# Kernel tuning notes

Measured on AMD Instinct MI355X. Metric: run time of the kernel, lower is better.

The kernel has to match this reference:

```python
import jax, jax.numpy as jnp
import numpy as np
import math

N_NODES = 64000
N_GRAPHS = 512
HIDDEN = 128
CLUSTERS = 10
NUM_FILTER = 16
N_CLASSES = 2
S_HID = math.ceil((HIDDEN + CLUSTERS) / 2)  # 69
P_HID = 8


def _mlp2(x, w1, b1, w2, b2):
    # 2-layer MLP: Linear -> ReLU -> Linear (matches MLP(2, in, hid, out))
    return jax.nn.relu(x @ w1 + b1) @ w2 + b2


def setup_inputs() -> dict:
    key = jax.random.key(0)
    ks = jax.random.split(key, 12)
    # node embeddings (output of get_emb)
    H_all = jax.random.normal(ks[0], (N_NODES, HIDDEN), dtype=jnp.float32)
    # graph indicator: 125 nodes per graph, sorted (as produced by batching)
    batch = jnp.repeat(jnp.arange(N_GRAPHS, dtype=jnp.int32), N_NODES // N_GRAPHS)
    targets = jax.random.randint(ks[1], (N_GRAPHS,), 0, N_CLASSES, dtype=jnp.int32)
    s = 0.05
    # S_mlp: hidden -> S_HID -> clusters
    w1 = jax.random.normal(ks[2], (HIDDEN, S_HID), dtype=jnp.float32) * s
    b1 = jnp.zeros((S_HID,), dtype=jnp.float32)
    w2 = jax.random.normal(ks[3], (S_HID, CLUSTERS), dtype=jnp.float32) * s
    b2 = jnp.zeros((CLUSTERS,), dtype=jnp.float32)
    # final: hidden*clusters -> 2
    wf = jax.random.normal(ks[4], (HIDDEN * CLUSTERS, N_CLASSES), dtype=jnp.float32) * s
    bf = jnp.zeros((N_CLASSES,), dtype=jnp.float32)
    # prototype_features_MLP: hidden -> 8 -> num_graph_filter
    p1 = jax.random.normal(ks[5], (HIDDEN, P_HID), dtype=jnp.float32) * s
    pb1 = jnp.zeros((P_HID,), dtype=jnp.float32)
    p2 = jax.random.normal(ks[6], (P_HID, NUM_FILTER), dtype=jnp.float32) * s
    pb2 = jnp.zeros((NUM_FILTER,), dtype=jnp.float32)
    # correlation parameters (initialized like the torch module)
    corr_inter = jax.nn.softmax(jax.random.uniform(ks[7], (N_CLASSES, NUM_FILTER)), axis=0)
    corr_intra = jax.nn.softmax(jax.random.uniform(ks[8], (N_CLASSES, NUM_FILTER)), axis=1)
    return {"H_all": H_all, "batch": batch, "targets": targets,
            "w1": w1, "b1": b1, "w2": w2, "b2": b2,
            "wf": wf, "bf": bf,
            "p1": p1, "pb1": pb1, "p2": p2, "pb2": pb2,
            "corr_inter": corr_inter, "corr_intra": corr_intra}


def reference(H_all, batch, targets, w1, b1, w2, b2, wf, bf,
              p1, pb1, p2, pb2, corr_inter, corr_intra):
    # per-node soft cluster assignment  [N, C]
    S_all = jax.nn.softmax(_mlp2(H_all, w1, b1, w2, b2), axis=-1)
    # segment matmul E_g = S_g^T @ H_g  -> [B, C, D] via segment-reduced outer products
    outer = S_all[:, :, None] * H_all[:, None, :]  # [N, C, D]
    E_all = jax.ops.segment_sum(outer, batch, num_segments=N_GRAPHS)
    B = E_all.shape[0]
    pred1 = E_all.reshape(B, -1) @ wf + bf  # dropout off (eval)
    p = jax.nn.softmax(pred1, axis=-1)
    # multinomial sample from pred_softmax (no grad)
    key = jax.random.key(42)
    sample = jax.random.categorical(key, jnp.log(jax.lax.stop_gradient(p) + 1e-12), axis=-1)
    ind_positive_sample = sample == targets
    oh = jax.nn.one_hot(sample, N_CLASSES, dtype=p.dtype)
    epsilon = jax.lax.stop_gradient(jnp.where(oh != 0, 1.0 - p, -p))
    sample_cat_oh = p + epsilon  # straight-through one-hot
    Q = jax.nn.softmax(_mlp2(E_all, p1, pb1, p2, pb2), axis=-1)  # [B, C, F]
    correlation = jax.nn.softmax(corr_inter, axis=0) * jax.nn.softmax(corr_intra, axis=1)  # [2, F]
    correlation_mask = sample_cat_oh @ correlation  # [B, F]
    feature_mask = jnp.sum(Q * correlation_mask[:, None, :], axis=-1)  # [B, C]
    E_masked = feature_mask[:, :, None] * E_all  # einsum('bi,bij->bij')
    pred2 = E_masked.reshape(B, -1) @ wf + bf
    return (pred1, pred2, ind_positive_sample, S_all, E_all, Q)
```

## Files before the change

### kernel.cpp

```cpp
#include <hip/hip_runtime.h>

#define NN 64000
#define NG 512
#define NPG 125
#define DIM 128
#define NC 10
#define SHID 69
#define NF 16
#define PHID 8
#define ELPAD 132
#define TSTR 85
#define PSTR 41

#define OFF_PRED1 0
#define OFF_PRED2 1024
#define OFF_IND   2048
#define OFF_S     2560
#define OFF_E     642560
#define OFF_Q     1297920

typedef __attribute__((ext_vector_type(8))) short short8;
typedef __attribute__((ext_vector_type(4))) float f32x4;

__device__ __forceinline__ unsigned rotl32(unsigned x, int r) {
    return (x << r) | (x >> (32 - r));
}

__device__ __forceinline__ void threefry_0_42(unsigned x0, unsigned x1,
                                              unsigned& o0, unsigned& o1) {
    const unsigned k0 = 0u, k1 = 42u;
    const unsigned k2 = k0 ^ k1 ^ 0x1BD11BDAu;
    unsigned ks[3] = {k0, k1, k2};
    const int R0[4] = {13, 15, 26, 6};
    const int R1[4] = {17, 29, 16, 24};
    x0 += k0; x1 += k1;
    #pragma unroll
    for (int i = 0; i < 5; i++) {
        const int* R = (i & 1) ? R1 : R0;
        #pragma unroll
        for (int r = 0; r < 4; r++) {
            x0 += x1;
            x1 = rotl32(x1, R[r]);
            x1 ^= x0;
        }
        x0 += ks[(i + 1) % 3];
        x1 += ks[(i + 2) % 3] + (unsigned)(i + 1);
    }
    o0 = x0; o1 = x1;
}

__device__ __forceinline__ unsigned random_bits_partitionable(unsigned i) {
    unsigned o0, o1;
    threefry_0_42(0u, i, o0, o1);
    return o0 ^ o1;
}

__device__ __forceinline__ float gumbel_from_bits(unsigned bits) {
    float f = __uint_as_float((bits >> 9) | 0x3f800000u) - 1.0f;
    if (f <= 0.0f) f = 1.1754943508222875e-38f;
    return -logf(-logf(f));
}

#define R10(M) M(0) M(1) M(2) M(3) M(4) M(5) M(6) M(7) M(8) M(9)

__global__ __launch_bounds__(256, 4) void k_node_mlp(
    const float* __restrict__ H, const float* __restrict__ w1,
    const float* __restrict__ b1, const float* __restrict__ w2,
    const float* __restrict__ b2, float* __restrict__ S) {
    __shared__ __align__(16) char lds[40960];
    short* fragHi = (short*)lds;
    short* fragLo = (short*)(lds + 20480);
    int tid = threadIdx.x;

    for (int s = tid; s < 1280; s += 256) {
        int jt = s >> 8, ks = (s >> 6) & 3, l = s & 63;
        int j = jt * 16 + (l & 15);
        int kb = ks * 32 + ((l >> 4) & 3) * 8;
        short8 vh, vl;
        #pragma unroll
        for (int i = 0; i < 8; i++) {
            float x = (j < SHID) ? w1[(kb + i) * SHID + j] : 0.0f;
            unsigned u = __float_as_uint(x);
            vh[i] = (short)(u >> 16);
            float hf = __uint_as_float(u & 0xFFFF0000u);
            float lo = x - hf;
            vl[i] = (short)(__float_as_uint(lo) >> 16);
        }
        *(short8*)(fragHi + (size_t)s * 8) = vh;
        *(short8*)(fragLo + (size_t)s * 8) = vl;
    }
    __syncthreads();

    int w = tid >> 6, l = tid & 63;
    int node = blockIdx.x * 64 + w * 16 + (l & 15);
    const float* Hp = H + (size_t)node * DIM + ((l >> 4) & 3) * 8;

    short8 aHi[4], aLo[4];
    #pragma unroll
    for (int ks = 0; ks < 4; ks++) {
        float4 x0 = *(const float4*)(Hp + ks * 32);
        float4 x1 = *(const float4*)(Hp + ks * 32 + 4);
        float xs[8] = {x0.x, x0.y, x0.z, x0.w, x1.x, x1.y, x1.z, x1.w};
        #pragma unroll
        for (int i = 0; i < 8; i++) {
            unsigned u = __float_as_uint(xs[i]);
            aHi[ks][i] = (short)(u >> 16);
            float lo = xs[i] - __uint_as_float(u & 0xFFFF0000u);
            aLo[ks][i] = (short)(__float_as_uint(lo) >> 16);
        }
    }

    f32x4 acc[5];
    #pragma unroll
    for (int jt = 0; jt < 5; jt++) {
        f32x4 a = {0.f, 0.f, 0.f, 0.f};
        #pragma unroll
        for (int ks = 0; ks < 4; ks++) {
            int slot = (jt * 4 + ks) * 64 + l;
            short8 bh = *(short8*)(fragHi + (size_t)slot * 8);
            short8 bl = *(short8*)(fragLo + (size_t)slot * 8);
            a = __builtin_amdgcn_mfma_f32_16x16x32_bf16(aHi[ks], bh, a, 0, 0, 0);
            a = __builtin_amdgcn_mfma_f32_16x16x32_bf16(aLo[ks], bh, a, 0, 0, 0);
            a = __builtin_amdgcn_mfma_f32_16x16x32_bf16(aHi[ks], bl, a, 0, 0, 0);
        }
        acc[jt] = a;
    }
    __syncthreads();

    float* Ts = (float*)lds;
    float* Ps = (float*)(lds + 21760);
    #pragma unroll
    for (int jt = 0; jt < 5; jt++) {
        int j = jt * 16 + (l & 15);
        float bj = (j < SHID) ? b1[j] : 0.0f;
        #pragma unroll
        for (int r = 0; r < 4; r++) {
            int m = w * 16 + ((l >> 4) & 3) * 4 + r;
            float tv = acc[jt][r];
            Ts[m * TSTR + j] = (j < SHID) ? fmaxf(tv + bj, 0.0f) : 0.0f;
        }
    }
    __syncthreads();

    {
        int n = tid & 63, q = tid >> 6;
        float lg[NC] = {};
        for (int jj = 0; jj < 18; jj++) {
            int j = q * 18 + jj;
            int jx = (j < SHID) ? j : (SHID - 1);
            float tr = Ts[n * TSTR + j];
            const float* w2r = w2 + jx * NC;
            #pragma unroll
            for (int c = 0; c < NC; c++) lg[c] = fmaf(tr, w2r[c], lg[c]);
        }
        #pragma unroll
        for (int c = 0; c < NC; c++) Ps[n * PSTR + q * NC + c] = lg[c];
    }
    __syncthreads();

    if (tid < 64) {
        int n = tid;
        const float* pr = &Ps[n * PSTR];
        #define LD(c) float s##c = pr[c] + pr[10 + c] + pr[20 + c] + pr[30 + c] + b2[c];
        R10(LD)
        #undef LD
        float m = fmaxf(fmaxf(fmaxf(s0, s1), fmaxf(s2, s3)),
                        fmaxf(fmaxf(fmaxf(s4, s5), fmaxf(s6, s7)), fmaxf(s8, s9)));
        float e0 = expf(s0 - m), e1 = expf(s1 - m), e2 = expf(s2 - m),
              e3 = expf(s3 - m), e4 = expf(s4 - m), e5 = expf(s5 - m),
              e6 = expf(s6 - m), e7 = expf(s7 - m), e8 = expf(s8 - m),
              e9 = expf(s9 - m);
        float ssum = ((e0 + e1) + (e2 + e3)) + ((e4 + e5) + (e6 + e7)) + (e8 + e9);
        float inv = 1.0f / ssum;
        float2* Sp2 = (float2*)(S + ((size_t)blockIdx.x * 64 + n) * NC);
        Sp2[0] = make_float2(e0 * inv, e1 * inv);
        Sp2[1] = make_float2(e2 * inv, e3 * inv);
        Sp2[2] = make_float2(e4 * inv, e5 * inv);
        Sp2[3] = make_float2(e6 * inv, e7 * inv);
        Sp2[4] = make_float2(e8 * inv, e9 * inv);
    }
}

__global__ __launch_bounds__(512, 2) void k_E_tail(
    const float* __restrict__ H, const float* __restrict__ S,
    const float* __restrict__ wf, const float* __restrict__ bf,
    const int* __restrict__ targets,
    const float* __restrict__ p1, const float* __restrict__ pb1,
    const float* __restrict__ p2, const float* __restrict__ pb2,
    const float* __restrict__ ci, const float* __restrict__ cr,
    float* __restrict__ E, float* __restrict__ pred1, float* __restrict__ pred2,
    float* __restrict__ ind, float* __restrict__ Q) {
    __shared__ __align__(8) float Sl[128 * NC];
    __shared__ float Epart[3 * 128 * NC];
    __shared__ __align__(16) float El[NC * ELPAD];
    __shared__ float fmbuf[NC];
    int g = blockIdx.x, tid = threadIdx.x;

    const float* Sg = S + (size_t)g * NPG * NC;
    for (int i = tid; i < 128 * NC; i += 512) Sl[i] = (i < NPG * NC) ? Sg[i] : 0.0f;
    __syncthreads();

    int q = tid >> 7;
    int d = tid & 127;
    const float* Hg = H + (size_t)g * NPG * DIM + d;

    #define DECLA(c) float a##c = 0.f;
    R10(DECLA)
    #undef DECLA
    int n0 = q * 32;
    #pragma unroll
    for (int ib = 0; ib < 32; ib += 4) {
        float h[4];
        #pragma unroll
        for (int u = 0; u < 4; u++) {
            int nh = min(n0 + ib + u, NPG - 1);
            h[u] = Hg[(size_t)nh * DIM];
        }
        #pragma unroll
        for (int u = 0; u < 4; u++) {
            const float2* S2 = (const float2*)(Sl + (n0 + ib + u) * NC);
            float2 s01 = S2[0], s23 = S2[1], s45 = S2[2], s67 = S2[3], s89 = S2[4];
            a0 = fmaf(s01.x, h[u], a0); a1 = fmaf(s01.y, h[u], a1);
            a2 = fmaf(s23.x, h[u], a2); a3 = fmaf(s23.y, h[u], a3);
            a4 = fmaf(s45.x, h[u], a4); a5 = fmaf(s45.y, h[u], a5);
            a6 = fmaf(s67.x, h[u], a6); a7 = fmaf(s67.y, h[u], a7);
            a8 = fmaf(s89.x, h[u], a8); a9 = fmaf(s89.y, h[u], a9);
        }
    }
    if (q > 0) {
        float* ep = &Epart[(q - 1) * 128 * NC + d * NC];
        #define STP(c) ep[c] = a##c;
        R10(STP)
        #undef STP
    }
    __syncthreads();
    if (q == 0) {
        const float* e1p = &Epart[d * NC];
        const float* e2p = &Epart[128 * NC + d * NC];
        const float* e3p = &Epart[2 * 128 * NC + d * NC];
        float* Eo = E + (size_t)g * (NC * DIM) + d;
        #define CMB(c) { a##c += e1p[c] + e2p[c] + e3p[c]; \
                         El[c * ELPAD + d] = a##c; Eo[c * DIM] = a##c; }
        R10(CMB)
        #undef CMB
    }
    __syncthreads();

    const float2* wf2 = (const float2*)wf;
    int l = tid;
    int samp = 0;
    float corr_lf = 0.f;

    if (tid < 64) {
        if (l < 32) {
            int i = l >> 4, f = l & 15;
            float a = ci[f], b = ci[NF + f];
            float mm = fmaxf(a, b);
            float ea = expf(a - mm), eb = expf(b - mm);
            float inter = expf(ci[i * NF + f] - mm) / (ea + eb);
            float mi = -1e30f;
            for (int j = 0; j < NF; j++) mi = fmaxf(mi, cr[i * NF + j]);
            float ri = 0.f;
            for (int j = 0; j < NF; j++) ri += expf(cr[i * NF + j] - mi);
            float intra = expf(cr[i * NF + f] - mi) / ri;
            corr_lf = inter * intra;
        }

        float a0 = 0.f, a1 = 0.f;
        #pragma unroll
        for (int i = 0; i < 20; i++) {
            int idx = i * 64 + l;
            float e = El[(idx >> 7) * ELPAD + (idx & 127)];
            float2 w = wf2[idx];
            a0 = fmaf(e, w.x, a0);
            a1 = fmaf(e, w.y, a1);
        }
        #pragma unroll
        for (int off = 32; off > 0; off >>= 1) {
            a0 += __shfl_down(a0, off);
            a1 += __shfl_down(a1, off);
        }
        if (l == 0) {
            float y0 = a0 + bf[0], y1 = a1 + bf[1];
            pred1[g * 2] = y0;
            pred1[g * 2 + 1] = y1;
            float m = fmaxf(y0, y1);
            float e0 = expf(y0 - m), e1 = expf(y1 - m), s = e0 + e1;
            float p0 = e0 / s, pp1 = e1 / s;
            float g0 = gumbel_from_bits(random_bits_partitionable(2 * g));
            float g1 = gumbel_from_bits(random_bits_partitionable(2 * g + 1));
            float l0 = logf(p0 + 1e-12f) + g0;
            float l1 = logf(pp1 + 1e-12f) + g1;
            samp = (l1 > l0) ? 1 : 0;
            ind[g] = (samp == targets[g]) ? 1.0f : 0.0f;
        }
        samp = __shfl(samp, 0);

        if (l < 40) {
            int p = l >> 2, s = l & 3;
            float ua = pb1[2 * s], ub = pb1[2 * s + 1];
            const float4* E4 = (const float4*)&El[p * ELPAD];
            #pragma unroll 4
            for (int k4 = 0; k4 < 32; k4++) {
                float4 e4 = E4[k4];
                float es[4] = {e4.x, e4.y, e4.z, e4.w};
                #pragma unroll
                for (int kk = 0; kk < 4; kk++) {
                    int k = k4 * 4 + kk;
                    ua = fmaf(es[kk], p1[k * PHID + 2 * s], ua);
                    ub = fmaf(es[kk], p1[k * PHID + 2 * s + 1], ub);
                }
            }
            ua = fmaxf(ua, 0.f);
            ub = fmaxf(ub, 0.f);
            float v[NF];
            #pragma unroll
            for (int f = 0; f < NF; f++) {
                v[f] = pb2[f] * 0.25f;
                v[f] = fmaf(ua, p2[(2 * s) * NF + f], v[f]);
                v[f] = fmaf(ub, p2[(2 * s + 1) * NF + f], v[f]);
            }
            #pragma unroll
            for (int f = 0; f < NF; f++) {
                v[f] += __shfl_xor(v[f], 1);
                v[f] += __shfl_xor(v[f], 2);
            }
            float m = v[0];
            #pragma unroll
            for (int f = 1; f < NF; f++) m = fmaxf(m, v[f]);
            float ssum = 0.f, qv[NF];
            #pragma unroll
            for (int f = 0; f < NF; f++) { qv[f] = expf(v[f] - m); ssum += qv[f]; }
            float inv = 1.0f / ssum;
            #pragma unroll
            for (int f = 0; f < NF; f++) qv[f] *= inv;
            float* Qo = Q + ((size_t)g * NC + p) * NF;
            ((float4*)Qo)[s] = make_float4(qv[s * 4], qv[s * 4 + 1], qv[s * 4 + 2], qv[s * 4 + 3]);
            float fmv = 0.f;
            #pragma unroll
            for (int f = 0; f < NF; f++) {
                float cv = __shfl(corr_lf, samp * NF + f);
                fmv = fmaf(qv[f], cv, fmv);
            }
            if (s == 0) fmbuf[p] = fmv;
        }
    }
    __syncthreads();

    if (tid < 64) {
        float b0 = 0.f, b1acc = 0.f;
        #pragma unroll
        for (int i = 0; i < 20; i++) {
            int idx = i * 64 + l;
            float e = El[(idx >> 7) * ELPAD + (idx & 127)] * fmbuf[idx >> 7];
            float2 w = wf2[idx];
            b0 = fmaf(e, w.x, b0);
            b1acc = fmaf(e, w.y, b1acc);
        }
        #pragma unroll
        for (int off = 32; off > 0; off >>= 1) {
            b0 += __shfl_down(b0, off);
            b1acc += __shfl_down(b1acc, off);
        }
        if (l == 0) {
            pred2[g * 2] = b0 + bf[0];
            pred2[g * 2 + 1] = b1acc + bf[1];
        }
    }
}

extern "C" void kernel_launch(void* const* d_in, const int* in_sizes, int n_in,
                              void* d_out, int out_size, void* d_ws, size_t ws_size,
                              hipStream_t stream) {
    const float* H       = (const float*)d_in[0];
    const int*   targets = (const int*)d_in[2];
    const float* w1      = (const float*)d_in[3];
    const float* b1      = (const float*)d_in[4];
    const float* w2      = (const float*)d_in[5];
    const float* b2      = (const float*)d_in[6];
    const float* wf      = (const float*)d_in[7];
    const float* bf      = (const float*)d_in[8];
    const float* p1      = (const float*)d_in[9];
    const float* pb1     = (const float*)d_in[10];
    const float* p2      = (const float*)d_in[11];
    const float* pb2     = (const float*)d_in[12];
    const float* ci      = (const float*)d_in[13];
    const float* cr      = (const float*)d_in[14];

    float* out   = (float*)d_out;
    float* pred1 = out + OFF_PRED1;
    float* pred2 = out + OFF_PRED2;
    float* ind   = out + OFF_IND;
    float* S     = out + OFF_S;
    float* E     = out + OFF_E;
    float* Q     = out + OFF_Q;

    k_node_mlp<<<NN / 64, 256, 0, stream>>>(H, w1, b1, w2, b2, S);
    k_E_tail<<<NG, 512, 0, stream>>>(H, S, wf, bf, targets, p1, pb1, p2, pb2,
                                     ci, cr, E, pred1, pred2, ind, Q);
}
```

Measured before the change: 126.9 us.

## Fuse node MLP with per-graph segment sum and precompute split w1 fragments

Merges the per-node S MLP kernel into the per-graph kernel so each block computes S for its 125 nodes, keeps S in LDS, and then forms E without re-reading S from global memory. The bf16 hi/lo split of w1 now runs once in a small pre-kernel that writes to workspace, and each block copies the prepared fragments into LDS. This removes the S round trip and one launch gap, and H is reused across both phases. In exchange, blocks shrink from 512 to 256 threads, LDS per block grows, occupancy drops, and the pre-kernel adds a launch.

```diff
diff --git a/kernel.cpp b/kernel.cpp
--- a/kernel.cpp
+++ b/kernel.cpp
@@ -9,8 +9,8 @@
 #define NF 16
 #define PHID 8
 #define ELPAD 132
-#define TSTR 85
-#define PSTR 41
+#define TSTR 81
+#define PSTR 21
 
 #define OFF_PRED1 0
 #define OFF_PRED2 1024
@@ -63,191 +63,221 @@
 
 #define R10(M) M(0) M(1) M(2) M(3) M(4) M(5) M(6) M(7) M(8) M(9)
 
-__global__ __launch_bounds__(256, 4) void k_node_mlp(
-    const float* __restrict__ H, const float* __restrict__ w1,
+__global__ void k_split_w1(const float* __restrict__ w1, short* __restrict__ ws) {
+    int e = blockIdx.x * 256 + threadIdx.x;
+    int slot = e >> 3, i = e & 7;
+    int jt = slot >> 8, ks = (slot >> 6) & 3, l = slot & 63;
+    int j = jt * 16 + (l & 15);
+    int kb = ks * 32 + ((l >> 4) & 3) * 8;
+    float x = (j < SHID) ? w1[(kb + i) * SHID + j] : 0.0f;
+    unsigned u = __float_as_uint(x);
+    short hi = (short)(u >> 16);
+    float hf = __uint_as_float(u & 0xFFFF0000u);
+    short lo = (short)(__float_as_uint(x - hf) >> 16);
+    ws[e] = hi;
+    ws[10240 + e] = lo;
+}
+
+__global__ __launch_bounds__(256, 2) void k_fused(
+    const float* __restrict__ H, const short* __restrict__ ws,
     const float* __restrict__ b1, const float* __restrict__ w2,
-    const float* __restrict__ b2, float* __restrict__ S) {
-    __shared__ __align__(16) char lds[40960];
-    short* fragHi = (short*)lds;
-    short* fragLo = (short*)(lds + 20480);
-    int tid = threadIdx.x;
-
-    for (int s = tid; s < 1280; s += 256) {
-        int jt = s >> 8, ks = (s >> 6) & 3, l = s & 63;
-        int j = jt * 16 + (l & 15);
-        int kb = ks * 32 + ((l >> 4) & 3) * 8;
-        short8 vh, vl;
-        #pragma unroll
-        for (int i = 0; i < 8; i++) {
-            float x = (j < SHID) ? w1[(kb + i) * SHID + j] : 0.0f;
-            unsigned u = __float_as_uint(x);
-            vh[i] = (short)(u >> 16);
-            float hf = __uint_as_float(u & 0xFFFF0000u);
-            float lo = x - hf;
-            vl[i] = (short)(__float_as_uint(lo) >> 16);
-        }
-        *(short8*)(fragHi + (size_t)s * 8) = vh;
-        *(short8*)(fragLo + (size_t)s * 8) = vl;
-    }
-    __syncthreads();
-
-    int w = tid >> 6, l = tid & 63;
-    int node = blockIdx.x * 64 + w * 16 + (l & 15);
-    const float* Hp = H + (size_t)node * DIM + ((l >> 4) & 3) * 8;
-
-    short8 aHi[4], aLo[4];
-    #pragma unroll
-    for (int ks = 0; ks < 4; ks++) {
-        float4 x0 = *(const float4*)(Hp + ks * 32);
-        float4 x1 = *(const float4*)(Hp + ks * 32 + 4);
-        float xs[8] = {x0.x, x0.y, x0.z, x0.w, x1.x, x1.y, x1.z, x1.w};
-        #pragma unroll
-        for (int i = 0; i < 8; i++) {
-            unsigned u = __float_as_uint(xs[i]);
-            aHi[ks][i] = (short)(u >> 16);
-            float lo = xs[i] - __uint_as_float(u & 0xFFFF0000u);
-            aLo[ks][i] = (short)(__float_as_uint(lo) >> 16);
-        }
-    }
-
-    f32x4 acc[5];
-    #pragma unroll
-    for (int jt = 0; jt < 5; jt++) {
-        f32x4 a = {0.f, 0.f, 0.f, 0.f};
-        #pragma unroll
-        for (int ks = 0; ks < 4; ks++) {
-            int slot = (jt * 4 + ks) * 64 + l;
-            short8 bh = *(short8*)(fragHi + (size_t)slot * 8);
-            short8 bl = *(short8*)(fragLo + (size_t)slot * 8);
-            a = __builtin_amdgcn_mfma_f32_16x16x32_bf16(aHi[ks], bh, a, 0, 0, 0);
-            a = __builtin_amdgcn_mfma_f32_16x16x32_bf16(aLo[ks], bh, a, 0, 0, 0);
-            a = __builtin_amdgcn_mfma_f32_16x16x32_bf16(aHi[ks], bl, a, 0, 0, 0);
-        }
-        acc[jt] = a;
-    }
-    __syncthreads();
-
-    float* Ts = (float*)lds;
-    float* Ps = (float*)(lds + 21760);
-    #pragma unroll
-    for (int jt = 0; jt < 5; jt++) {
-        int j = jt * 16 + (l & 15);
-        float bj = (j < SHID) ? b1[j] : 0.0f;
-        #pragma unroll
-        for (int r = 0; r < 4; r++) {
-            int m = w * 16 + ((l >> 4) & 3) * 4 + r;
-            float tv = acc[jt][r];
-            Ts[m * TSTR + j] = (j < SHID) ? fmaxf(tv + bj, 0.0f) : 0.0f;
-        }
-    }
-    __syncthreads();
-
-    {
-        int n = tid & 63, q = tid >> 6;
-        float lg[NC] = {};
-        for (int jj = 0; jj < 18; jj++) {
-            int j = q * 18 + jj;
-            int jx = (j < SHID) ? j : (SHID - 1);
-            float tr = Ts[n * TSTR + j];
-            const float* w2r = w2 + jx * NC;
-            #pragma unroll
-            for (int c = 0; c < NC; c++) lg[c] = fmaf(tr, w2r[c], lg[c]);
-        }
-        #pragma unroll
-        for (int c = 0; c < NC; c++) Ps[n * PSTR + q * NC + c] = lg[c];
-    }
-    __syncthreads();
-
-    if (tid < 64) {
-        int n = tid;
-        const float* pr = &Ps[n * PSTR];
-        #define LD(c) float s##c = pr[c] + pr[10 + c] + pr[20 + c] + pr[30 + c] + b2[c];
-        R10(LD)
-        #undef LD
-        float m = fmaxf(fmaxf(fmaxf(s0, s1), fmaxf(s2, s3)),
-                        fmaxf(fmaxf(fmaxf(s4, s5), fmaxf(s6, s7)), fmaxf(s8, s9)));
-        float e0 = expf(s0 - m), e1 = expf(s1 - m), e2 = expf(s2 - m),
-              e3 = expf(s3 - m), e4 = expf(s4 - m), e5 = expf(s5 - m),
-              e6 = expf(s6 - m), e7 = expf(s7 - m), e8 = expf(s8 - m),
-              e9 = expf(s9 - m);
-        float ssum = ((e0 + e1) + (e2 + e3)) + ((e4 + e5) + (e6 + e7)) + (e8 + e9);
-        float inv = 1.0f / ssum;
-        float2* Sp2 = (float2*)(S + ((size_t)blockIdx.x * 64 + n) * NC);
-        Sp2[0] = make_float2(e0 * inv, e1 * inv);
-        Sp2[1] = make_float2(e2 * inv, e3 * inv);
-        Sp2[2] = make_float2(e4 * inv, e5 * inv);
-        Sp2[3] = make_float2(e6 * inv, e7 * inv);
-        Sp2[4] = make_float2(e8 * inv, e9 * inv);
-    }
-}
-
-__global__ __launch_bounds__(512, 2) void k_E_tail(
-    const float* __restrict__ H, const float* __restrict__ S,
+    const float* __restrict__ b2,
     const float* __restrict__ wf, const float* __restrict__ bf,
     const int* __restrict__ targets,
     const float* __restrict__ p1, const float* __restrict__ pb1,
     const float* __restrict__ p2, const float* __restrict__ pb2,
     const float* __restrict__ ci, const float* __restrict__ cr,
-    float* __restrict__ E, float* __restrict__ pred1, float* __restrict__ pred2,
+    float* __restrict__ S, float* __restrict__ E,
+    float* __restrict__ pred1, float* __restrict__ pred2,
     float* __restrict__ ind, float* __restrict__ Q) {
-    __shared__ __align__(8) float Sl[128 * NC];
-    __shared__ float Epart[3 * 128 * NC];
-    __shared__ __align__(16) float El[NC * ELPAD];
-    __shared__ float fmbuf[NC];
+    __shared__ __align__(16) char lds[57600];
     int g = blockIdx.x, tid = threadIdx.x;
 
-    const float* Sg = S + (size_t)g * NPG * NC;
-    for (int i = tid; i < 128 * NC; i += 512) Sl[i] = (i < NPG * NC) ? Sg[i] : 0.0f;
-    __syncthreads();
-
-    int q = tid >> 7;
-    int d = tid & 127;
-    const float* Hg = H + (size_t)g * NPG * DIM + d;
-
-    #define DECLA(c) float a##c = 0.f;
-    R10(DECLA)
-    #undef DECLA
-    int n0 = q * 32;
+    {
+        const float4* src = (const float4*)ws;
+        float4* dst = (float4*)lds;
+        #pragma unroll
+        for (int k = 0; k < 10; k++) dst[k * 256 + tid] = src[k * 256 + tid];
+    }
+    short* fragHi = (short*)lds;
+    short* fragLo = (short*)(lds + 20480);
+    __syncthreads();
+
+    int w = tid >> 6, l = tid & 63;
+
+    short8 aHi[2][4], aLo[2][4];
     #pragma unroll
-    for (int ib = 0; ib < 32; ib += 4) {
-        float h[4];
-        #pragma unroll
-        for (int u = 0; u < 4; u++) {
-            int nh = min(n0 + ib + u, NPG - 1);
-            h[u] = Hg[(size_t)nh * DIM];
-        }
-        #pragma unroll
-        for (int u = 0; u < 4; u++) {
-            const float2* S2 = (const float2*)(Sl + (n0 + ib + u) * NC);
-            float2 s01 = S2[0], s23 = S2[1], s45 = S2[2], s67 = S2[3], s89 = S2[4];
-            a0 = fmaf(s01.x, h[u], a0); a1 = fmaf(s01.y, h[u], a1);
-            a2 = fmaf(s23.x, h[u], a2); a3 = fmaf(s23.y, h[u], a3);
-            a4 = fmaf(s45.x, h[u], a4); a5 = fmaf(s45.y, h[u], a5);
-            a6 = fmaf(s67.x, h[u], a6); a7 = fmaf(s67.y, h[u], a7);
-            a8 = fmaf(s89.x, h[u], a8); a9 = fmaf(s89.y, h[u], a9);
-        }
-    }
-    if (q > 0) {
-        float* ep = &Epart[(q - 1) * 128 * NC + d * NC];
-        #define STP(c) ep[c] = a##c;
-        R10(STP)
-        #undef STP
-    }
-    __syncthreads();
-    if (q == 0) {
-        const float* e1p = &Epart[d * NC];
-        const float* e2p = &Epart[128 * NC + d * NC];
-        const float* e3p = &Epart[2 * 128 * NC + d * NC];
-        float* Eo = E + (size_t)g * (NC * DIM) + d;
-        #define CMB(c) { a##c += e1p[c] + e2p[c] + e3p[c]; \
-                         El[c * ELPAD + d] = a##c; Eo[c * DIM] = a##c; }
-        R10(CMB)
-        #undef CMB
+    for (int h = 0; h < 2; h++) {
+        int r = (w * 2 + h) * 16 + (l & 15);
+        bool valid = (r < NPG);
+        const float* Hp = H + ((size_t)g * NPG + (valid ? r : 0)) * DIM + ((l >> 4) & 3) * 8;
+        #pragma unroll
+        for (int ks = 0; ks < 4; ks++) {
+            float xs[8];
+            if (valid) {
+                float4 x0 = *(const float4*)(Hp + ks * 32);
+                float4 x1 = *(const float4*)(Hp + ks * 32 + 4);
+                xs[0] = x0.x; xs[1] = x0.y; xs[2] = x0.z; xs[3] = x0.w;
+                xs[4] = x1.x; xs[5] = x1.y; xs[6] = x1.z; xs[7] = x1.w;
+            } else {
+                #pragma unroll
+                for (int i = 0; i < 8; i++) xs[i] = 0.0f;
+            }
+            #pragma unroll
+            for (int i = 0; i < 8; i++) {
+                unsigned u = __float_as_uint(xs[i]);
+                aHi[h][ks][i] = (short)(u >> 16);
+                float lo = xs[i] - __uint_as_float(u & 0xFFFF0000u);
+                aLo[h][ks][i] = (short)(__float_as_uint(lo) >> 16);
+            }
+        }
+    }
+
+    f32x4 acc[2][5];
+    #pragma unroll
+    for (int h = 0; h < 2; h++)
+        #pragma unroll
+        for (int jt = 0; jt < 5; jt++) acc[h][jt] = (f32x4){0.f, 0.f, 0.f, 0.f};
+    #pragma unroll
+    for (int jt = 0; jt < 5; jt++) {
+        #pragma unroll
+        for (int ks = 0; ks < 4; ks++) {
+            int slot = (jt * 4 + ks) * 64 + l;
+            short8 bh = *(short8*)(fragHi + (size_t)slot * 8);
+            short8 bl = *(short8*)(fragLo + (size_t)slot * 8);
+            acc[0][jt] = __builtin_amdgcn_mfma_f32_16x16x32_bf16(aHi[0][ks], bh, acc[0][jt], 0, 0, 0);
+            acc[1][jt] = __builtin_amdgcn_mfma_f32_16x16x32_bf16(aHi[1][ks], bh, acc[1][jt], 0, 0, 0);
+            acc[0][jt] = __builtin_amdgcn_mfma_f32_16x16x32_bf16(aLo[0][ks], bh, acc[0][jt], 0, 0, 0);
+            acc[1][jt] = __builtin_amdgcn_mfma_f32_16x16x32_bf16(aLo[1][ks], bh, acc[1][jt], 0, 0, 0);
+            acc[0][jt] = __builtin_amdgcn_mfma_f32_16x16x32_bf16(aHi[0][ks], bl, acc[0][jt], 0, 0, 0);
+            acc[1][jt] = __builtin_amdgcn_mfma_f32_16x16x32_bf16(aHi[1][ks], bl, acc[1][jt], 0, 0, 0);
+        }
+    }
+    __syncthreads();
+
+    float* Ts = (float*)lds;
+    #pragma unroll
+    for (int jt = 0; jt < 5; jt++) {
+        int j = jt * 16 + (l & 15);
+        float bj = (j < SHID) ? b1[j] : 0.0f;
+        #pragma unroll
+        for (int h = 0; h < 2; h++) {
+            #pragma unroll
+            for (int r = 0; r < 4; r++) {
+                int m = (w * 2 + h) * 16 + ((l >> 4) & 3) * 4 + r;
+                float tv = acc[h][jt][r];
+                Ts[m * TSTR + j] = (j < SHID) ? fmaxf(tv + bj, 0.0f) : 0.0f;
+            }
+        }
+    }
+    __syncthreads();
+
+    float* Ps = (float*)(lds + 41472);
+    {
+        int n = tid & 127, q = tid >> 7;
+        float lg[NC] = {};
+        for (int jj = 0; jj < 36; jj++) {
+            int j = q * 36 + jj;
+            int jx = (j < SHID) ? j : (SHID - 1);
+            float tr = Ts[n * TSTR + j];
+            const float* w2r = w2 + jx * NC;
+            #pragma unroll
+            for (int c = 0; c < NC; c++) lg[c] = fmaf(tr, w2r[c], lg[c]);
+        }
+        #pragma unroll
+        for (int c = 0; c < NC; c++) Ps[n * PSTR + q * NC + c] = lg[c];
+    }
+    __syncthreads();
+
+    float* Ss = (float*)(lds + 52224);
+    if (tid < 128) {
+        int n = tid;
+        if (n < NPG) {
+            const float* pr = &Ps[n * PSTR];
+            #define LD(c) float s##c = pr[c] + pr[NC + c] + b2[c];
+            R10(LD)
+            #undef LD
+            float m = fmaxf(fmaxf(fmaxf(s0, s1), fmaxf(s2, s3)),
+                            fmaxf(fmaxf(fmaxf(s4, s5), fmaxf(s6, s7)), fmaxf(s8, s9)));
+            float e0 = expf(s0 - m), e1 = expf(s1 - m), e2 = expf(s2 - m),
+                  e3 = expf(s3 - m), e4 = expf(s4 - m), e5 = expf(s5 - m),
+                  e6 = expf(s6 - m), e7 = expf(s7 - m), e8 = expf(s8 - m),
+                  e9 = expf(s9 - m);
+            float ssum = ((e0 + e1) + (e2 + e3)) + ((e4 + e5) + (e6 + e7)) + (e8 + e9);
+            float inv = 1.0f / ssum;
+            float v0 = e0 * inv, v1 = e1 * inv, v2 = e2 * inv, v3 = e3 * inv,
+                  v4 = e4 * inv, v5 = e5 * inv, v6 = e6 * inv, v7 = e7 * inv,
+                  v8 = e8 * inv, v9 = e9 * inv;
+            float2* Sp2 = (float2*)(S + ((size_t)g * NPG + n) * NC);
+            Sp2[0] = make_float2(v0, v1);
+            Sp2[1] = make_float2(v2, v3);
+            Sp2[2] = make_float2(v4, v5);
+            Sp2[3] = make_float2(v6, v7);
+            Sp2[4] = make_float2(v8, v9);
+            float2* Ss2 = (float2*)(Ss + n * NC);
+            Ss2[0] = make_float2(v0, v1);
+            Ss2[1] = make_float2(v2, v3);
+            Ss2[2] = make_float2(v4, v5);
+            Ss2[3] = make_float2(v6, v7);
+            Ss2[4] = make_float2(v8, v9);
+        } else {
+            float2* Ss2 = (float2*)(Ss + n * NC);
+            Ss2[0] = make_float2(0.f, 0.f);
+            Ss2[1] = make_float2(0.f, 0.f);
+            Ss2[2] = make_float2(0.f, 0.f);
+            Ss2[3] = make_float2(0.f, 0.f);
+            Ss2[4] = make_float2(0.f, 0.f);
+        }
+    }
+    __syncthreads();
+
+    float* Epart = (float*)lds;
+    float* El    = (float*)(lds + 8192);
+    float* fmbuf = (float*)(lds + 16384);
+    {
+        int q = tid >> 7, d = tid & 127;
+        const float* Hg = H + (size_t)g * NPG * DIM + d;
+        #define DECLA(c) float a##c = 0.f;
+        R10(DECLA)
+        #undef DECLA
+        int n0 = q * 64;
+        #pragma unroll
+        for (int ib = 0; ib < 64; ib += 4) {
+            float h4[4];
+            #pragma unroll
+            for (int u = 0; u < 4; u++) {
+                int nh = min(n0 + ib + u, NPG - 1);
+                h4[u] = Hg[(size_t)nh * DIM];
+            }
+            #pragma unroll
+            for (int u = 0; u < 4; u++) {
+                const float2* S2 = (const float2*)(Ss + (n0 + ib + u) * NC);
+                float2 s01 = S2[0], s23 = S2[1], s45 = S2[2], s67 = S2[3], s89 = S2[4];
+                a0 = fmaf(s01.x, h4[u], a0); a1 = fmaf(s01.y, h4[u], a1);
+                a2 = fmaf(s23.x, h4[u], a2); a3 = fmaf(s23.y, h4[u], a3);
+                a4 = fmaf(s45.x, h4[u], a4); a5 = fmaf(s45.y, h4[u], a5);
+                a6 = fmaf(s67.x, h4[u], a6); a7 = fmaf(s67.y, h4[u], a7);
+                a8 = fmaf(s89.x, h4[u], a8); a9 = fmaf(s89.y, h4[u], a9);
+            }
+        }
+        if (q == 1) {
+            float* ep = &Epart[d * NC];
+            #define STP(c) ep[c] = a##c;
+            R10(STP)
+            #undef STP
+        }
+        __syncthreads();
+        if (q == 0) {
+            const float* ep = &Epart[d * NC];
+            float* Eo = E + (size_t)g * (NC * DIM) + d;
+            #define CMB(c) { a##c += ep[c]; El[c * ELPAD + d] = a##c; Eo[c * DIM] = a##c; }
+            R10(CMB)
+            #undef CMB
+        }
     }
     __syncthreads();
 
     const float2* wf2 = (const float2*)wf;
-    int l = tid;
     int samp = 0;
     float corr_lf = 0.f;
 
@@ -271,9 +301,9 @@
         for (int i = 0; i < 20; i++) {
             int idx = i * 64 + l;
             float e = El[(idx >> 7) * ELPAD + (idx & 127)];
-            float2 w = wf2[idx];
-            a0 = fmaf(e, w.x, a0);
-            a1 = fmaf(e, w.y, a1);
+            float2 wv = wf2[idx];
+            a0 = fmaf(e, wv.x, a0);
+            a1 = fmaf(e, wv.y, a1);
         }
         #pragma unroll
         for (int off = 32; off > 0; off >>= 1) {
@@ -353,9 +383,9 @@
         for (int i = 0; i < 20; i++) {
             int idx = i * 64 + l;
             float e = El[(idx >> 7) * ELPAD + (idx & 127)] * fmbuf[idx >> 7];
-            float2 w = wf2[idx];
-            b0 = fmaf(e, w.x, b0);
-            b1acc = fmaf(e, w.y, b1acc);
+            float2 wv = wf2[idx];
+            b0 = fmaf(e, wv.x, b0);
+            b1acc = fmaf(e, wv.y, b1acc);
         }
         #pragma unroll
         for (int off = 32; off > 0; off >>= 1) {
@@ -395,7 +425,10 @@
     float* E     = out + OFF_E;
     float* Q     = out + OFF_Q;
 
-    k_node_mlp<<<NN / 64, 256, 0, stream>>>(H, w1, b1, w2, b2, S);
-    k_E_tail<<<NG, 512, 0, stream>>>(H, S, wf, bf, targets, p1, pb1, p2, pb2,
-                                     ci, cr, E, pred1, pred2, ind, Q);
-}
+    short* ws = (short*)d_ws;
+
+    k_split_w1<<<40, 256, 0, stream>>>(w1, ws);
+    k_fused<<<NG, 256, 0, stream>>>(H, ws, b1, w2, b2, wf, bf, targets,
+                                    p1, pb1, p2, pb2, ci, cr,
+                                    S, E, pred1, pred2, ind, Q);
+}
```

Result: no change. 125.6 us (-1.0%).
